# Kernel optimization log

Hardware: AMD Instinct MI355X
Metric: run time of the kernel (lower is better)

The kernel has to match this reference:

```python
import jax, jax.numpy as jnp
import numpy as np


def _fdiff(a, axis):
    """conv3d with forward-difference kernel and padding=1 along `axis`:
    out[i] = a[i+1] - a[i] for i < L-1, out[L-1] = -a[L-1]. Same length as input."""
    d = jnp.diff(a, axis=axis)
    L = a.shape[axis]
    last = -jax.lax.slice_in_dim(a, L - 1, L, axis=axis)
    return jnp.concatenate([d, last], axis=axis)


def correlation_3d(prev, nxt):
    """FunctionCorrelation_3D: 27-channel local cost volume.
    Faithful to the source: the z 'shift' loop only zero-masks the prev edge slice
    (identical slicing on both sides of the += in the original), then a 9-channel
    3x3 (x,y) displacement correlation (mean over channels) is taken vs next.
    Output: [B, 27, X, Y, Z], channel order = k (z) outer, (dx, dy) inner."""
    B, C, X, Y, Z = prev.shape
    nxt_p = jnp.pad(nxt, ((0, 0), (0, 0), (1, 1), (1, 1), (0, 0)))
    outs = []
    for k in (-1, 0, 1):
        zmask = jnp.ones((Z,), prev.dtype)
        if k == -1:
            zmask = zmask.at[Z - 1].set(0.0)
        elif k == 1:
            zmask = zmask.at[0].set(0.0)
        pm = prev * zmask  # broadcast over last axis
        for dx in (-1, 0, 1):
            for dy in (-1, 0, 1):
                ns = nxt_p[:, :, 1 + dx:1 + dx + X, 1 + dy:1 + dy + Y, :]
                outs.append(jnp.mean(pm * ns, axis=1))  # [B, X, Y, Z]
    return jnp.stack(outs, axis=1)  # [B, 27, X, Y, Z]


def cgrid_to_motion(u, v, w, Hc, Wc, Tc):
    mu = (u[:, :, 1:-1, 1:-1, 1:] + u[:, :, 1:-1, 1:-1, :-1]) * 0.5
    mv = (v[:, :, 1:-1, 1:, 1:-1] + v[:, :, 1:-1, :-1, 1:-1]) * 0.5
    mw = (w[:, :, 1:, 1:-1, 1:-1] + w[:, :, :-1, 1:-1, 1:-1]) * 0.5
    m = jnp.concatenate([mu, mv, mw], axis=1)  # [B, 3, X-2, Y-2, Z-2]
    up = (m.shape[2] - Hc) // 2
    left = (m.shape[3] - Wc) // 2
    front = (m.shape[4] - Tc) // 2
    return m[:, :, up:up + Hc, left:left + Wc, front:front + Tc]


def calc_phi_velocity(phi, Hc, Wc, Tc):
    # staggered C-grid gradient; the [:-1] slice on each staggered axis turns the
    # padded forward-difference conv into a plain diff along that axis.
    u = jnp.diff(phi, axis=4)  # [B,1,X,Y,Z-1]
    v = jnp.diff(phi, axis=3)  # [B,1,X,Y-1,Z]
    w = jnp.diff(phi, axis=2)  # [B,1,X-1,Y,Z]
    return cgrid_to_motion(u, v, w, Hc, Wc, Tc)


def calc_stream_velocity(stream, Hc, Wc, Tc):
    s0 = stream[:, 0:1]
    s1 = stream[:, 1:2]
    s2 = stream[:, 2:3]
    u = (_fdiff(s1, 2) - _fdiff(s0, 3))[..., :-1]          # staggered on z
    v = (_fdiff(s0, 4) - _fdiff(s2, 2))[:, :, :, :-1, :]    # staggered on y
    w = (_fdiff(s2, 3) - _fdiff(s1, 4))[:, :, :-1, :, :]    # staggered on x
    return cgrid_to_motion(u, v, w, Hc, Wc, Tc)


def setup_inputs() -> dict:
    key = jax.random.key(0)
    k1, k2, k3, k4 = jax.random.split(key, 4)
    B, C, X = 8, 32, 48
    H = 96
    return {
        "prev_feat": jax.random.normal(k1, (B, C, X, X, X), jnp.float32),
        "next_feat": jax.random.normal(k2, (B, C, X, X, X), jnp.float32),
        "phi": jax.random.normal(k3, (B, 1, H, H, H), jnp.float32),
        "stream": jax.random.normal(k4, (B, 3, H, H, H), jnp.float32),
        "out_h": 94,
        "out_w": 94,
        "out_t": 94,
    }


def reference(prev_feat, next_feat, phi, stream, out_h, out_w, out_t):
    corr = correlation_3d(prev_feat, next_feat)
    vel_phi = calc_phi_velocity(phi, out_h, out_w, out_t)
    vel_stream = calc_stream_velocity(stream, out_h, out_w, out_t)
    vel = vel_phi + vel_stream
    return (corr, vel, vel_phi, vel_stream)
```

## Files before the change

### kernel.cpp

```cpp
#include <hip/hip_runtime.h>


typedef float f2 __attribute__((ext_vector_type(2)));

constexpr int CB = 8, CC = 32, CX = 48, CY = 48, CZ = 48;
constexpr int H = 96, O = 94;

constexpr int CORR_NWG = (CB * CX * CY * (CZ / 2)) / 256;
constexpr int VEL_TOTAL = CB * O * O * (O / 2);
constexpr int VEL_NWG = (VEL_TOTAL + 255) / 256;

__device__ __forceinline__ void corr_body(
    int bid, const float* __restrict__ prev, const float* __restrict__ nxt,
    float* __restrict__ corr)
{
    constexpr int Z2 = CZ / 2;
    int swz = (bid & 7) * (CORR_NWG / 8) + (bid >> 3);
    int idx = swz * 256 + (int)threadIdx.x;
    int z2 = idx % Z2; int r = idx / Z2;
    int y = r % CY; r /= CY;
    int x = r % CX; int b = r / CX;

    const int plane = CY * CZ;
    const int cstr  = CX * plane;
    const size_t bbase = (size_t)b * CC * cstr;

    const float* pp = prev + bbase + (size_t)x * plane + (size_t)y * CZ + z2 * 2;

    const float* tpx[3];
    bool okx[3], oky[3];
#pragma unroll
    for (int d = 0; d < 3; ++d) {
        int xx = x + d - 1;
        okx[d] = (unsigned)xx < (unsigned)CX;
        tpx[d] = nxt + bbase + (size_t)(okx[d] ? xx : x) * plane
                             + (size_t)y * CZ + z2 * 2;
        int yy = y + d - 1;
        oky[d] = (unsigned)yy < (unsigned)CY;
    }
    bool okj[9];
#pragma unroll
    for (int a = 0; a < 3; ++a)
#pragma unroll
        for (int dyy = 0; dyy < 3; ++dyy) okj[a * 3 + dyy] = okx[a] && oky[dyy];

    f2 acc[9];
#pragma unroll
    for (int jj = 0; jj < 9; ++jj) acc[jj] = f2{0.f, 0.f};

#pragma unroll 2
    for (int c = 0; c < CC; ++c) {
        f2 pv = *reinterpret_cast<const f2*>(pp);
#pragma unroll
        for (int a = 0; a < 3; ++a) {
#pragma unroll
            for (int dyy = 0; dyy < 3; ++dyy) {
                const int jj = a * 3 + dyy;
                if (okj[jj]) {
                    f2 nv = *reinterpret_cast<const f2*>(tpx[a] + (dyy - 1) * CZ);
                    acc[jj] += pv * nv;
                }
            }
            tpx[a] += cstr;
        }
        pp += cstr;
    }

    const size_t obase = (size_t)b * 27 * cstr + (size_t)x * plane
                       + (size_t)y * CZ + z2 * 2;
    const float s = 1.0f / 32.0f;
#pragma unroll
    for (int jj = 0; jj < 9; ++jj) {
        f2 v = acc[jj] * s;
        f2 gm = v; if (z2 == Z2 - 1) gm.y = 0.f;
        f2 gp = v; if (z2 == 0)      gp.x = 0.f;
        __builtin_nontemporal_store(gm, (f2*)(corr + obase + (size_t)jj * cstr));
        __builtin_nontemporal_store(v,  (f2*)(corr + obase + (size_t)(9 + jj) * cstr));
        __builtin_nontemporal_store(gp, (f2*)(corr + obase + (size_t)(18 + jj) * cstr));
    }
}

__device__ __forceinline__ void vel_body(
    int bid, const float* __restrict__ phi, const float* __restrict__ stm,
    float* __restrict__ vel, float* __restrict__ vphi, float* __restrict__ vstr)
{
    constexpr int TT = O / 2;
    const int q = VEL_NWG >> 3, rr = VEL_NWG & 7;
    int xcd = bid & 7, g = bid >> 3;
    int swz = (xcd < rr) ? (xcd * (q + 1) + g) : (rr * (q + 1) + (xcd - rr) * q + g);
    int idx = swz * 256 + (int)threadIdx.x;
    if (idx >= VEL_TOTAL) return;
    int tt = idx % TT; int r2 = idx / TT;
    int j = r2 % O; r2 /= O;
    int i = r2 % O; int b = r2 / O;
    const int t = tt * 2;

    const int hp = H * H;
    const size_t hc = (size_t)H * hp;
    const float* ph = phi + (size_t)b * hc;
    const float* s0 = stm + (size_t)b * 3 * hc;
    const float* s1 = s0 + hc;
    const float* s2 = s1 + hc;

#define R(A, B_) ((size_t)(A) * hp + (size_t)(B_) * H + t)

    const float* p11 = ph + R(i + 1, j + 1);
    f2 p11a = *(const f2*)p11;
    f2 p11b = *(const f2*)(p11 + 2);
    float p12_1 = ph[R(i + 1, j + 2) + 1], p12_2 = ph[R(i + 1, j + 2) + 2];
    float p10_1 = ph[R(i + 1, j)     + 1], p10_2 = ph[R(i + 1, j)     + 2];
    float p21_1 = ph[R(i + 2, j + 1) + 1], p21_2 = ph[R(i + 2, j + 1) + 2];
    float p01_1 = ph[R(i,     j + 1) + 1], p01_2 = ph[R(i,     j + 1) + 2];

    float pc0 = p11a.y, pc1 = p11b.x;
    float mup0 = ((p11b.x - pc0) + (pc0 - p11a.x)) * 0.5f;
    float mup1 = ((p11b.y - pc1) + (pc1 - p11a.y)) * 0.5f;
    float mvp0 = ((p12_1 - pc0) + (pc0 - p10_1)) * 0.5f;
    float mvp1 = ((p12_2 - pc1) + (pc1 - p10_2)) * 0.5f;
    float mwp0 = ((p21_1 - pc0) + (pc0 - p01_1)) * 0.5f;
    float mwp1 = ((p21_2 - pc1) + (pc1 - p01_2)) * 0.5f;

    const float* q1_11 = s1 + R(i + 1, j + 1);
    f2 s1_11a = *(const f2*)q1_11;  f2 s1_11b = *(const f2*)(q1_11 + 2);
    const float* q1_21 = s1 + R(i + 2, j + 1);
    f2 s1_21a = *(const f2*)q1_21;  float s1_21_2 = q1_21[2];
    const float* q1_01 = s1 + R(i, j + 1);
    float s1_01_1 = q1_01[1];       f2 s1_01b = *(const f2*)(q1_01 + 2);

    const float* q0_11 = s0 + R(i + 1, j + 1);
    f2 s0_11a = *(const f2*)q0_11;  f2 s0_11b = *(const f2*)(q0_11 + 2);
    const float* q0_12 = s0 + R(i + 1, j + 2);
    f2 s0_12a = *(const f2*)q0_12;  float s0_12_2 = q0_12[2];
    const float* q0_10 = s0 + R(i + 1, j);
    float s0_10_1 = q0_10[1];       f2 s0_10b = *(const f2*)(q0_10 + 2);

    float s2_21_1 = s2[R(i + 2, j + 1) + 1], s2_21_2 = s2[R(i + 2, j + 1) + 2];
    float s2_11_1 = s2[R(i + 1, j + 1) + 1], s2_11_2 = s2[R(i + 1, j + 1) + 2];
    float s2_20_1 = s2[R(i + 2, j)     + 1], s2_20_2 = s2[R(i + 2, j)     + 2];
    float s2_10_1 = s2[R(i + 1, j)     + 1], s2_10_2 = s2[R(i + 1, j)     + 2];
    float s2_12_1 = s2[R(i + 1, j + 2) + 1], s2_12_2 = s2[R(i + 1, j + 2) + 2];
    float s2_02_1 = s2[R(i,     j + 2) + 1], s2_02_2 = s2[R(i,     j + 2) + 2];
    float s2_01_1 = s2[R(i,     j + 1) + 1], s2_01_2 = s2[R(i,     j + 1) + 2];
#undef R

    float u0 = (s1_21a.x - s1_11a.x) - (s0_12a.x - s0_11a.x);
    float u1 = (s1_21a.y - s1_11a.y) - (s0_12a.y - s0_11a.y);
    float u2 = (s1_21_2  - s1_11b.x) - (s0_12_2  - s0_11b.x);
    float mus0 = (u1 + u0) * 0.5f;
    float mus1 = (u2 + u1) * 0.5f;

    float v1_0 = (s0_11b.x - s0_11a.y) - (s2_21_1 - s2_11_1);
    float v0_0 = (s0_10b.x - s0_10_1)  - (s2_20_1 - s2_10_1);
    float mvs0 = (v1_0 + v0_0) * 0.5f;
    float v1_1 = (s0_11b.y - s0_11b.x) - (s2_21_2 - s2_11_2);
    float v0_1 = (s0_10b.y - s0_10b.x) - (s2_20_2 - s2_10_2);
    float mvs1 = (v1_1 + v0_1) * 0.5f;

    float w1_0 = (s2_12_1 - s2_11_1) - (s1_11b.x - s1_11a.y);
    float w0_0 = (s2_02_1 - s2_01_1) - (s1_01b.x - s1_01_1);
    float mws0 = (w1_0 + w0_0) * 0.5f;
    float w1_1 = (s2_12_2 - s2_11_2) - (s1_11b.y - s1_11b.x);
    float w0_1 = (s2_02_2 - s2_01_2) - (s1_01b.y - s1_01b.x);
    float mws1 = (w1_1 + w0_1) * 0.5f;

    const size_t oc = (size_t)O * O * O;
    const size_t o  = ((size_t)i * O + j) * O + t;
    const size_t b3 = (size_t)b * 3;
    __builtin_nontemporal_store(f2{mup0, mup1}, (f2*)(vphi + (b3 + 0) * oc + o));
    __builtin_nontemporal_store(f2{mvp0, mvp1}, (f2*)(vphi + (b3 + 1) * oc + o));
    __builtin_nontemporal_store(f2{mwp0, mwp1}, (f2*)(vphi + (b3 + 2) * oc + o));
    __builtin_nontemporal_store(f2{mus0, mus1}, (f2*)(vstr + (b3 + 0) * oc + o));
    __builtin_nontemporal_store(f2{mvs0, mvs1}, (f2*)(vstr + (b3 + 1) * oc + o));
    __builtin_nontemporal_store(f2{mws0, mws1}, (f2*)(vstr + (b3 + 2) * oc + o));
    __builtin_nontemporal_store(f2{mup0 + mus0, mup1 + mus1}, (f2*)(vel + (b3 + 0) * oc + o));
    __builtin_nontemporal_store(f2{mvp0 + mvs0, mvp1 + mvs1}, (f2*)(vel + (b3 + 1) * oc + o));
    __builtin_nontemporal_store(f2{mwp0 + mws0, mwp1 + mws1}, (f2*)(vel + (b3 + 2) * oc + o));
}

__global__ __launch_bounds__(256) void fused_kernel(
    const float* __restrict__ prev, const float* __restrict__ nxt,
    const float* __restrict__ phi, const float* __restrict__ stm,
    float* __restrict__ corr, float* __restrict__ vel,
    float* __restrict__ vphi, float* __restrict__ vstr)
{
    int bid = blockIdx.x;
    if (bid < CORR_NWG) {
        corr_body(bid, prev, nxt, corr);
    } else {
        vel_body(bid - CORR_NWG, phi, stm, vel, vphi, vstr);
    }
}

extern "C" void kernel_launch(void* const* d_in, const int* in_sizes, int n_in,
                              void* d_out, int out_size, void* d_ws, size_t ws_size,
                              hipStream_t stream)
{
    const float* prev = (const float*)d_in[0];
    const float* nxt  = (const float*)d_in[1];
    const float* phi  = (const float*)d_in[2];
    const float* stm  = (const float*)d_in[3];

    float* out = (float*)d_out;
    const size_t corr_sz = (size_t)CB * 27 * CX * CY * CZ;
    const size_t vel_sz  = (size_t)CB * 3 * O * O * O;
    float* corr = out;
    float* vel  = out + corr_sz;
    float* vphi = vel + vel_sz;
    float* vstr = vphi + vel_sz;

    fused_kernel<<<CORR_NWG + VEL_NWG, 256, 0, stream>>>(
        prev, nxt, phi, stm, corr, vel, vphi, vstr);
}
```

Measured before the change: 208.7 us.

## Software-pipeline channel loads in correlation loop with branchless clamped offsets

The correlation loop now prefetches the next channel's prev and nine neighbour values while accumulating the current channel, and the loop is fully unrolled. Out-of-bounds neighbours are handled without branches by clamping the offset to a valid address and zeroing a per-neighbour scale factor at the end. The launch bounds also gain a minimum-occupancy hint of 6. The aim is to hide global load latency and remove divergent branches. In exchange it raises register pressure, and the occupancy hint may force spilling.

```diff
diff --git a/kernel.cpp b/kernel.cpp
--- a/kernel.cpp
+++ b/kernel.cpp
@@ -5,6 +5,8 @@
 
 constexpr int CB = 8, CC = 32, CX = 48, CY = 48, CZ = 48;
 constexpr int H = 96, O = 94;
+constexpr int PLANE = CY * CZ;
+constexpr int CSTR  = CX * PLANE;
 
 constexpr int CORR_NWG = (CB * CX * CY * (CZ / 2)) / 256;
 constexpr int VEL_TOTAL = CB * O * O * (O / 2);
@@ -21,62 +23,70 @@
     int y = r % CY; r /= CY;
     int x = r % CX; int b = r / CX;
 
-    const int plane = CY * CZ;
-    const int cstr  = CX * plane;
-    const size_t bbase = (size_t)b * CC * cstr;
-
-    const float* pp = prev + bbase + (size_t)x * plane + (size_t)y * CZ + z2 * 2;
-
-    const float* tpx[3];
-    bool okx[3], oky[3];
-#pragma unroll
-    for (int d = 0; d < 3; ++d) {
-        int xx = x + d - 1;
-        okx[d] = (unsigned)xx < (unsigned)CX;
-        tpx[d] = nxt + bbase + (size_t)(okx[d] ? xx : x) * plane
-                             + (size_t)y * CZ + z2 * 2;
-        int yy = y + d - 1;
-        oky[d] = (unsigned)yy < (unsigned)CY;
-    }
-    bool okj[9];
-#pragma unroll
-    for (int a = 0; a < 3; ++a)
-#pragma unroll
-        for (int dyy = 0; dyy < 3; ++dyy) okj[a * 3 + dyy] = okx[a] && oky[dyy];
+    const size_t bbase = (size_t)b * CC * CSTR;
+    const float* __restrict__ pbase = prev + bbase;
+    const float* __restrict__ nbase = nxt + bbase;
+
+    const int off0 = x * PLANE + y * CZ + z2 * 2;
+    int offj[9];
+    float scj[9];
+#pragma unroll
+    for (int a = 0; a < 3; ++a) {
+        int xx = x + a - 1;
+        bool vx = (unsigned)xx < (unsigned)CX;
+#pragma unroll
+        for (int d = 0; d < 3; ++d) {
+            int yy = y + d - 1;
+            bool ok = vx && ((unsigned)yy < (unsigned)CY);
+            offj[a * 3 + d] = (ok ? xx : x) * PLANE + (ok ? yy : y) * CZ + z2 * 2;
+            scj[a * 3 + d] = ok ? (1.0f / 32.0f) : 0.0f;
+        }
+    }
 
     f2 acc[9];
 #pragma unroll
     for (int jj = 0; jj < 9; ++jj) acc[jj] = f2{0.f, 0.f};
 
-#pragma unroll 2
+    const float* pc = pbase;
+    const float* nc = nbase;
+    f2 pA = *reinterpret_cast<const f2*>(pc + off0);
+    f2 nA[9];
+#pragma unroll
+    for (int jj = 0; jj < 9; ++jj)
+        nA[jj] = *reinterpret_cast<const f2*>(nc + offj[jj]);
+
+#pragma unroll
     for (int c = 0; c < CC; ++c) {
-        f2 pv = *reinterpret_cast<const f2*>(pp);
-#pragma unroll
-        for (int a = 0; a < 3; ++a) {
-#pragma unroll
-            for (int dyy = 0; dyy < 3; ++dyy) {
-                const int jj = a * 3 + dyy;
-                if (okj[jj]) {
-                    f2 nv = *reinterpret_cast<const f2*>(tpx[a] + (dyy - 1) * CZ);
-                    acc[jj] += pv * nv;
-                }
-            }
-            tpx[a] += cstr;
+        const float* pn = pc + CSTR;
+        const float* nn = nc + CSTR;
+        f2 pB = f2{0.f, 0.f};
+        f2 nB[9];
+#pragma unroll
+        for (int jj = 0; jj < 9; ++jj) nB[jj] = f2{0.f, 0.f};
+        if (c < CC - 1) {
+            pB = *reinterpret_cast<const f2*>(pn + off0);
+#pragma unroll
+            for (int jj = 0; jj < 9; ++jj)
+                nB[jj] = *reinterpret_cast<const f2*>(nn + offj[jj]);
         }
-        pp += cstr;
-    }
-
-    const size_t obase = (size_t)b * 27 * cstr + (size_t)x * plane
+#pragma unroll
+        for (int jj = 0; jj < 9; ++jj) acc[jj] += pA * nA[jj];
+        pA = pB;
+#pragma unroll
+        for (int jj = 0; jj < 9; ++jj) nA[jj] = nB[jj];
+        pc = pn; nc = nn;
+    }
+
+    const size_t obase = (size_t)b * 27 * CSTR + (size_t)x * PLANE
                        + (size_t)y * CZ + z2 * 2;
-    const float s = 1.0f / 32.0f;
 #pragma unroll
     for (int jj = 0; jj < 9; ++jj) {
-        f2 v = acc[jj] * s;
+        f2 v = acc[jj] * scj[jj];
         f2 gm = v; if (z2 == Z2 - 1) gm.y = 0.f;
         f2 gp = v; if (z2 == 0)      gp.x = 0.f;
-        __builtin_nontemporal_store(gm, (f2*)(corr + obase + (size_t)jj * cstr));
-        __builtin_nontemporal_store(v,  (f2*)(corr + obase + (size_t)(9 + jj) * cstr));
-        __builtin_nontemporal_store(gp, (f2*)(corr + obase + (size_t)(18 + jj) * cstr));
+        __builtin_nontemporal_store(gm, (f2*)(corr + obase + (size_t)jj * CSTR));
+        __builtin_nontemporal_store(v,  (f2*)(corr + obase + (size_t)(9 + jj) * CSTR));
+        __builtin_nontemporal_store(gp, (f2*)(corr + obase + (size_t)(18 + jj) * CSTR));
     }
 }
 
@@ -177,7 +187,7 @@
     __builtin_nontemporal_store(f2{mwp0 + mws0, mwp1 + mws1}, (f2*)(vel + (b3 + 2) * oc + o));
 }
 
-__global__ __launch_bounds__(256) void fused_kernel(
+__global__ __launch_bounds__(256, 6) void fused_kernel(
     const float* __restrict__ prev, const float* __restrict__ nxt,
     const float* __restrict__ phi, const float* __restrict__ stm,
     float* __restrict__ corr, float* __restrict__ vel,
```

After: 218.4 us. 1.05x slower.
